# Optimization experiments

Hardware: AMD Instinct MI355X
Metric: run time of the kernel (lower is better)

## Reference

```python
import jax, jax.numpy as jnp
import numpy as np

B, C, N = 8, 3, 4096
NSAMPLE = 10
MLP = (64, 64)
# checkerboard re-gather pattern from the original module
INDS = np.array([0, 1, 2, 3, 2, 3, 4, 5, 4, 5, 6, 7, 6, 7, 8, 9])


def setup_inputs() -> dict:
    key = jax.random.key(0)
    k1, k2, k3 = jax.random.split(key, 3)
    pos = jax.random.normal(k1, (B, C, N), jnp.float32)
    w1 = jax.random.normal(k2, (MLP[0], 4 * C, 2, 2), jnp.float32) * 0.1  # Conv2d(12, mlp0, k=2)
    b1 = jnp.zeros((MLP[0],), jnp.float32)
    w2 = jax.random.normal(k3, (MLP[1], MLP[0]), jnp.float32) * 0.1       # Conv2d(mlp0, mlp1, k=1)
    b2 = jnp.zeros((MLP[1],), jnp.float32)
    return {"pos": pos, "w1": w1, "b1": b1, "w2": w2, "b2": b2}


def _squeeze_2x2_alt(x):
    # x: [B, N, c, 4, 4] -> [B, N, 4c, 2, 2] with channel order [a, d, b, c]
    a = x[..., 0::2, 0::2]  # (0,0) of each 2x2 block
    d = x[..., 1::2, 1::2]  # (1,1)
    b = x[..., 0::2, 1::2]  # (0,1)
    c = x[..., 1::2, 0::2]  # (1,0)
    return jnp.concatenate([a, d, b, c], axis=-3)


def reference(pos, w1, b1, w2, b2):
    Bn, Cn, Nn = pos.shape
    pos_t = pos.transpose(0, 2, 1)  # [B, N, C]
    # pairwise squared distances [B, N, N]
    sq = jnp.sum(pos_t * pos_t, axis=-1)
    d2 = sq[:, :, None] - 2.0 * jnp.einsum('bnc,bmc->bnm', pos_t, pos_t) + sq[:, None, :]
    _, idx = jax.lax.top_k(-d2, NSAMPLE)  # [B, N, K] nearest neighbors (self first)
    # grouping_operation: grouped[b,c,n,k] = pos[b,c,idx[b,n,k]]
    grouped = jax.vmap(lambda p, i: p[:, i])(pos, idx)  # [B, C, N, K]
    pg = grouped[..., INDS]                              # [B, C, N, 16]
    pg = pg.transpose(0, 2, 1, 3).reshape(Bn, Nn, Cn, 4, 4)  # [B, N, 3, 4, 4]
    sqz = _squeeze_2x2_alt(pg)                           # [B, N, 12, 2, 2]
    # Conv2d(12->mlp0, k=2, stride=1) over 2x2 spatial == full contraction
    h = jnp.einsum('bnchw,ochw->bno', sqz, w1) + b1      # [B, N, mlp0]
    out = jnp.einsum('bno,po->bnp', h, w2) + b2          # [B, N, mlp1]
    return out.transpose(0, 2, 1)                        # [B, mlp1, N]
```

## Files before the change

### kernel.cpp

```cpp
#include <hip/hip_runtime.h>
#include <math.h>

#define NPTS 4096
#define NSMP 10

typedef _Float16 half4 __attribute__((ext_vector_type(4)));
typedef _Float16 half8 __attribute__((ext_vector_type(8)));
typedef float f32x16 __attribute__((ext_vector_type(16)));

__global__ __launch_bounds__(256) void prep_kernel(
    const float* __restrict__ w1, const float* __restrict__ b1,
    const float* __restrict__ w2, const float* __restrict__ b2,
    float* __restrict__ wn, float* __restrict__ bb) {
  __shared__ float w1l[64 * 48];
  __shared__ float w2t[64 * 64];
  __shared__ float b1l[64];
  __shared__ float part[4][30][64];
  __shared__ float bpart[4][64];
  const int t = threadIdx.x, p = t & 63, grp = t >> 6, o0 = grp * 16;
  for (int idx = t; idx < 64 * 48; idx += 256) w1l[idx] = w1[idx];
  for (int idx = t; idx < 64 * 64; idx += 256) w2t[(idx & 63) * 64 + (idx >> 6)] = w2[idx];
  if (t < 64) b1l[t] = b1[t];
  __syncthreads();

  const int sg[16] = {0,2,4,6, 3,5,7,9, 1,3,5,7, 2,4,6,8};
  float w2r[16];
  #pragma unroll
  for (int oo = 0; oo < 16; ++oo) w2r[oo] = w2t[(o0 + oo) * 64 + p];
  float wloc[30];
  #pragma unroll
  for (int i = 0; i < 30; ++i) wloc[i] = 0.0f;
  #pragma unroll
  for (int g = 0; g < 4; ++g)
    #pragma unroll
    for (int i = 0; i < 2; ++i)
      #pragma unroll
      for (int j = 0; j < 2; ++j) {
        const int s = sg[g * 4 + i * 2 + j];
        #pragma unroll
        for (int c = 0; c < 3; ++c) {
          const int k = (c + 3 * g) * 4 + i * 2 + j;
          float wk = 0.0f;
          #pragma unroll
          for (int oo = 0; oo < 16; ++oo)
            wk = fmaf(w2r[oo], w1l[(o0 + oo) * 48 + k], wk);
          wloc[s * 3 + c] += wk;
        }
      }
  #pragma unroll
  for (int i = 0; i < 30; ++i) part[grp][i][p] = wloc[i];
  float sb = 0.0f;
  #pragma unroll
  for (int oo = 0; oo < 16; ++oo) sb = fmaf(w2r[oo], b1l[o0 + oo], sb);
  bpart[grp][p] = sb;
  __syncthreads();
  const float* p0 = &part[0][0][0];
  for (int idx = t; idx < 30 * 64; idx += 256)
    wn[idx] = p0[idx] + p0[1920 + idx] + p0[3840 + idx] + p0[5760 + idx];
  if (t < 64) bb[t] = b2[t] + bpart[0][t] + bpart[1][t] + bpart[2][t] + bpart[3][t];
}

__global__ __launch_bounds__(1024, 8) void topk_kernel(const float* __restrict__ pos,
                                                       const float* __restrict__ wng,
                                                       const float* __restrict__ bbg,
                                                       float* __restrict__ out) {
  __shared__ half4 pts4[NPTS];
  __shared__ float X[16 * 260];
  __shared__ half4 a4s[64];
  __shared__ float wl[30 * 64];
  __shared__ float bl[64];
  __shared__ float taub[64];
  __shared__ float sqqs[64];
  __shared__ int   cnt[64];
  __shared__ int   nbrT[64][NSMP];

  const int b = blockIdx.y, tid = threadIdx.x, lane = tid & 63, wv = tid >> 6;
  const float* pb = pos + (size_t)b * 3 * NPTS;
  const int nb = blockIdx.x * 64;

  for (int i = tid; i < NPTS; i += 1024) {
    float x = pb[i], y = pb[i + NPTS], z = pb[i + 2 * NPTS];
    float sq = fmaf(z, z, fmaf(y, y, x * x));
    half4 v = {(_Float16)x, (_Float16)y, (_Float16)z, (_Float16)sq};
    pts4[i] = v;
  }
  if (tid < 64) {
    float qx = pb[nb + tid], qy = pb[nb + tid + NPTS], qz = pb[nb + tid + 2 * NPTS];
    half4 va = {(_Float16)(-2.0f * (float)(_Float16)qx),
                (_Float16)(-2.0f * (float)(_Float16)qy),
                (_Float16)(-2.0f * (float)(_Float16)qz),
                (_Float16)1.0f};
    a4s[tid] = va;
    sqqs[tid] = fmaf(qz, qz, fmaf(qy, qy, qx * qx));
    cnt[tid] = 0;
    bl[tid] = bbg[tid];
  }
  for (int i = tid; i < 30 * 64; i += 1024) wl[i] = wng[i];
  __syncthreads();

  const int qt = wv >> 3, ws = wv & 7, h = lane >> 5, c31 = lane & 31;
  const int base = ws * 512;
  half8 af;
  #pragma unroll
  for (int j = 0; j < 8; ++j) af[j] = (_Float16)0.0f;
  {
    half4 aq = a4s[qt * 32 + c31];
    if (h == 0) { af[0] = aq[0]; af[1] = aq[1]; af[2] = aq[2]; af[3] = aq[3]; }
  }
  f32x16 zz;
  #pragma unroll
  for (int j = 0; j < 16; ++j) zz[j] = 0.0f;

  float mreg[16];
  #pragma unroll
  for (int j = 0; j < 16; ++j) mreg[j] = INFINITY;
  #pragma unroll 1
  for (int t = 0; t < 16; ++t) {
    half4 bp = pts4[base + t * 32 + c31];
    half8 bf;
    #pragma unroll
    for (int j = 0; j < 8; ++j) bf[j] = (_Float16)0.0f;
    bf[0] = bp[0]; bf[1] = bp[1]; bf[2] = bp[2]; bf[3] = bp[3];
    f32x16 acc = __builtin_amdgcn_mfma_f32_32x32x16_f16(af, bf, zz, 0, 0, 0);
    #pragma unroll
    for (int j = 0; j < 16; ++j) mreg[j] = fminf(mreg[j], acc[j]);
  }
  #pragma unroll
  for (int j = 0; j < 16; ++j) {
    mreg[j] = fminf(mreg[j], __shfl_xor(mreg[j], 1));
    mreg[j] = fminf(mreg[j], __shfl_xor(mreg[j], 2));
  }
  if ((lane & 3) == 0) {
    const int g = (lane >> 2) & 7;
    #pragma unroll
    for (int j = 0; j < 16; ++j) {
      const int row = qt * 32 + (j & 3) + 8 * (j >> 2) + 4 * h;
      X[row * 64 + ws * 8 + g] = mreg[j];
    }
  }
  __syncthreads();

  unsigned um[4];
  #pragma unroll
  for (int r = 0; r < 4; ++r) {
    float dm = X[(4 * wv + r) * 64 + lane];
    unsigned ub = __float_as_uint(dm);
    um[r] = (ub & 0x80000000u) ? ~ub : (ub | 0x80000000u);
  }
  unsigned pfx0 = 0u, pfx1 = 0u, pfx2 = 0u, pfx3 = 0u;
  #pragma unroll 1
  for (int bno = 31; bno >= 8; --bno) {
    const unsigned bit = 1u << bno, ones = bit - 1u;
    if (__popcll(__ballot(um[0] <= (pfx0 | ones))) < NSMP) pfx0 |= bit;
    if (__popcll(__ballot(um[1] <= (pfx1 | ones))) < NSMP) pfx1 |= bit;
    if (__popcll(__ballot(um[2] <= (pfx2 | ones))) < NSMP) pfx2 |= bit;
    if (__popcll(__ballot(um[3] <= (pfx3 | ones))) < NSMP) pfx3 |= bit;
  }
  float tx[4];
  #pragma unroll
  for (int r = 0; r < 4; ++r) {
    unsigned T = ((r == 0) ? pfx0 : (r == 1) ? pfx1 : (r == 2) ? pfx2 : pfx3) | 0xFFu;
    unsigned tb = (T & 0x80000000u) ? (T ^ 0x80000000u) : ~T;
    float tf = __uint_as_float(tb);
    float sqr = sqqs[4 * wv + r];
    float d10sq = tf + sqr;
    if (d10sq < 0.0f) d10sq = 0.0f;
    float aq = sqrtf(sqr);
    float L = aq + sqrtf(d10sq) + 0.05f;
    float slack = 2e-3f + 0.00146484375f * (4.0f * aq * L + L * L);
    tx[r] = __fadd_rn(tf, slack);
  }
  if (lane == 0) {
    taub[4 * wv + 0] = tx[0]; taub[4 * wv + 1] = tx[1];
    taub[4 * wv + 2] = tx[2]; taub[4 * wv + 3] = tx[3];
  }
  __syncthreads();

  float tau16[16];
  #pragma unroll
  for (int j = 0; j < 16; ++j) tau16[j] = taub[qt * 32 + (j & 3) + 8 * (j >> 2) + 4 * h];
  int* bufi = (int*)X;
  #pragma unroll 1
  for (int t = 0; t < 16; ++t) {
    const int m0 = base + t * 32 + c31;
    half4 bp = pts4[m0];
    half8 bf;
    #pragma unroll
    for (int j = 0; j < 8; ++j) bf[j] = (_Float16)0.0f;
    bf[0] = bp[0]; bf[1] = bp[1]; bf[2] = bp[2]; bf[3] = bp[3];
    f32x16 acc = __builtin_amdgcn_mfma_f32_32x32x16_f16(af, bf, zz, 0, 0, 0);
    #pragma unroll
    for (int j = 0; j < 16; ++j) {
      if (acc[j] <= tau16[j]) {
        const int row = qt * 32 + (j & 3) + 8 * (j >> 2) + 4 * h;
        int ps = atomicAdd(&cnt[row], 1);
        if (ps < 64) bufi[row * 64 + ps] = m0;
      }
    }
  }
  __syncthreads();

  int c[4], si[4], rank[4];
  double dd[4];
  int cmax = 0;
  #pragma unroll
  for (int r = 0; r < 4; ++r) {
    c[r] = __builtin_amdgcn_readfirstlane(cnt[4 * wv + r]);
    if (c[r] > 64) c[r] = 64;
    cmax = (c[r] > cmax) ? c[r] : cmax;
    rank[r] = 0;
  }
  #pragma unroll
  for (int r = 0; r < 4; ++r) {
    const int nq = nb + 4 * wv + r;
    float qxf = pb[nq], qyf = pb[nq + NPTS], qzf = pb[nq + 2 * NPTS];
    if (lane < c[r]) {
      si[r] = bufi[(4 * wv + r) * 64 + lane];
      float px = pb[si[r]], py = pb[si[r] + NPTS], pz = pb[si[r] + 2 * NPTS];
      double dqx = (double)qxf, dqy = (double)qyf, dqz = (double)qzf;
      double dpx = (double)px, dpy = (double)py, dpz = (double)pz;
      double dot = dqx * dpx + dqy * dpy + dqz * dpz;
      double sqn = dqx * dqx + dqy * dqy + dqz * dqz;
      double sqm = dpx * dpx + dpy * dpy + dpz * dpz;
      dd[r] = (sqn - 2.0 * dot) + sqm;
    } else { dd[r] = (double)INFINITY; si[r] = 0x7FFFFFFF; }
  }
  #pragma unroll 1
  for (int j = 0; j < cmax; ++j) {
    #pragma unroll
    for (int r = 0; r < 4; ++r) {
      int jlo = __builtin_amdgcn_readlane(__double2loint(dd[r]), j);
      int jhi = __builtin_amdgcn_readlane(__double2hiint(dd[r]), j);
      int ji  = __builtin_amdgcn_readlane(si[r], j);
      double jd = __hiloint2double(jhi, jlo);
      if (jd < dd[r] || (jd == dd[r] && ji < si[r])) ++rank[r];
    }
  }
  #pragma unroll
  for (int r = 0; r < 4; ++r)
    if (lane < c[r] && rank[r] < NSMP)
      nbrT[4 * wv + r][rank[r]] = si[r];
  __syncthreads();

  float* transF = &X[wv * 260];
  #pragma unroll 1
  for (int r = 0; r < 4; ++r) {
    float a = bl[lane];
    #pragma unroll
    for (int s = 0; s < NSMP; ++s) {
      const int id = nbrT[4 * wv + r][s];
      float px = pb[id], py = pb[id + NPTS], pz = pb[id + 2 * NPTS];
      a = fmaf(wl[(s * 3 + 0) * 64 + lane], px, a);
      a = fmaf(wl[(s * 3 + 1) * 64 + lane], py, a);
      a = fmaf(wl[(s * 3 + 2) * 64 + lane], pz, a);
    }
    transF[r * 65 + lane] = a;
  }
  __syncthreads();

  {
    int p = tid >> 4, t16 = tid & 15;
    float4 v;
    v.x = X[t16 * 260 + 0 * 65 + p];
    v.y = X[t16 * 260 + 1 * 65 + p];
    v.z = X[t16 * 260 + 2 * 65 + p];
    v.w = X[t16 * 260 + 3 * 65 + p];
    *(float4*)(out + ((size_t)b * 64 + p) * NPTS + nb + 4 * t16) = v;
  }
}

extern "C" void kernel_launch(void* const* d_in, const int* in_sizes, int n_in,
                              void* d_out, int out_size, void* d_ws, size_t ws_size,
                              hipStream_t stream) {
  (void)in_sizes; (void)n_in; (void)out_size; (void)ws_size;
  const float* pos = (const float*)d_in[0];
  const float* w1  = (const float*)d_in[1];
  const float* b1  = (const float*)d_in[2];
  const float* w2  = (const float*)d_in[3];
  const float* b2  = (const float*)d_in[4];
  float* out = (float*)d_out;

  float* wn = (float*)d_ws;
  float* bb = (float*)((char*)d_ws + 30 * 64 * 4);

  prep_kernel<<<dim3(1), dim3(256), 0, stream>>>(w1, b1, w2, b2, wn, bb);
  topk_kernel<<<dim3(64, 8), dim3(1024), 0, stream>>>(pos, wn, bb, out);
}
```

Measured before the change: 153.3 us.

## Switch distance MFMA from 32x32x16 to 16x16x32 with per-wave 16-query tiles

Replaces the 32x32x16 MFMA tiling of the query-by-point distance pass with 16x16x32 MFMAs. Each wave now covers 16 queries over a quarter of the points, with 64 iterations instead of 16, in both the min-reduction pass and the candidate collection pass. The per-lane column minimum is now written straight to a padded (stride 65) shared buffer, which drops the cross-lane shuffle reduction and is meant to reduce bank conflicts. The cost is four times as many smaller MFMA issues and more loop iterations. The minima layout changes from 8 per wave segment to 16 columns per segment, which also feeds the threshold radix search differently.

```diff
diff --git a/kernel.cpp b/kernel.cpp
--- a/kernel.cpp
+++ b/kernel.cpp
@@ -6,7 +6,7 @@
 
 typedef _Float16 half4 __attribute__((ext_vector_type(4)));
 typedef _Float16 half8 __attribute__((ext_vector_type(8)));
-typedef float f32x16 __attribute__((ext_vector_type(16)));
+typedef float f32x4 __attribute__((ext_vector_type(4)));
 
 __global__ __launch_bounds__(256) void prep_kernel(
     const float* __restrict__ w1, const float* __restrict__ b1,
@@ -98,52 +98,42 @@
   for (int i = tid; i < 30 * 64; i += 1024) wl[i] = wng[i];
   __syncthreads();
 
-  const int qt = wv >> 3, ws = wv & 7, h = lane >> 5, c31 = lane & 31;
-  const int base = ws * 512;
+  const int qt = wv >> 2, ws = wv & 3, g = lane >> 4, col = lane & 15;
+  const int base = ws * 1024;
+  const int rowb = qt * 16 + g * 4;
   half8 af;
   #pragma unroll
   for (int j = 0; j < 8; ++j) af[j] = (_Float16)0.0f;
-  {
-    half4 aq = a4s[qt * 32 + c31];
-    if (h == 0) { af[0] = aq[0]; af[1] = aq[1]; af[2] = aq[2]; af[3] = aq[3]; }
-  }
-  f32x16 zz;
-  #pragma unroll
-  for (int j = 0; j < 16; ++j) zz[j] = 0.0f;
-
-  float mreg[16];
-  #pragma unroll
-  for (int j = 0; j < 16; ++j) mreg[j] = INFINITY;
-  #pragma unroll 1
-  for (int t = 0; t < 16; ++t) {
-    half4 bp = pts4[base + t * 32 + c31];
+  if (g == 0) {
+    half4 aq = a4s[qt * 16 + col];
+    af[0] = aq[0]; af[1] = aq[1]; af[2] = aq[2]; af[3] = aq[3];
+  }
+  f32x4 zz;
+  #pragma unroll
+  for (int j = 0; j < 4; ++j) zz[j] = 0.0f;
+
+  float mreg[4];
+  #pragma unroll
+  for (int j = 0; j < 4; ++j) mreg[j] = INFINITY;
+  #pragma unroll 2
+  for (int t = 0; t < 64; ++t) {
+    half4 bp = pts4[base + t * 16 + col];
     half8 bf;
-    #pragma unroll
-    for (int j = 0; j < 8; ++j) bf[j] = (_Float16)0.0f;
     bf[0] = bp[0]; bf[1] = bp[1]; bf[2] = bp[2]; bf[3] = bp[3];
-    f32x16 acc = __builtin_amdgcn_mfma_f32_32x32x16_f16(af, bf, zz, 0, 0, 0);
-    #pragma unroll
-    for (int j = 0; j < 16; ++j) mreg[j] = fminf(mreg[j], acc[j]);
-  }
-  #pragma unroll
-  for (int j = 0; j < 16; ++j) {
-    mreg[j] = fminf(mreg[j], __shfl_xor(mreg[j], 1));
-    mreg[j] = fminf(mreg[j], __shfl_xor(mreg[j], 2));
-  }
-  if ((lane & 3) == 0) {
-    const int g = (lane >> 2) & 7;
-    #pragma unroll
-    for (int j = 0; j < 16; ++j) {
-      const int row = qt * 32 + (j & 3) + 8 * (j >> 2) + 4 * h;
-      X[row * 64 + ws * 8 + g] = mreg[j];
-    }
-  }
+    bf[4] = bp[0]; bf[5] = bp[1]; bf[6] = bp[2]; bf[7] = bp[3];
+    f32x4 acc = __builtin_amdgcn_mfma_f32_16x16x32_f16(af, bf, zz, 0, 0, 0);
+    #pragma unroll
+    for (int j = 0; j < 4; ++j) mreg[j] = fminf(mreg[j], acc[j]);
+  }
+  #pragma unroll
+  for (int j = 0; j < 4; ++j)
+    X[(rowb + j) * 65 + ws * 16 + col] = mreg[j];
   __syncthreads();
 
   unsigned um[4];
   #pragma unroll
   for (int r = 0; r < 4; ++r) {
-    float dm = X[(4 * wv + r) * 64 + lane];
+    float dm = X[(4 * wv + r) * 65 + lane];
     unsigned ub = __float_as_uint(dm);
     um[r] = (ub & 0x80000000u) ? ~ub : (ub | 0x80000000u);
   }
@@ -176,23 +166,22 @@
   }
   __syncthreads();
 
-  float tau16[16];
-  #pragma unroll
-  for (int j = 0; j < 16; ++j) tau16[j] = taub[qt * 32 + (j & 3) + 8 * (j >> 2) + 4 * h];
+  float tau4[4];
+  #pragma unroll
+  for (int j = 0; j < 4; ++j) tau4[j] = taub[rowb + j];
   int* bufi = (int*)X;
-  #pragma unroll 1
-  for (int t = 0; t < 16; ++t) {
-    const int m0 = base + t * 32 + c31;
+  #pragma unroll 2
+  for (int t = 0; t < 64; ++t) {
+    const int m0 = base + t * 16 + col;
     half4 bp = pts4[m0];
     half8 bf;
-    #pragma unroll
-    for (int j = 0; j < 8; ++j) bf[j] = (_Float16)0.0f;
     bf[0] = bp[0]; bf[1] = bp[1]; bf[2] = bp[2]; bf[3] = bp[3];
-    f32x16 acc = __builtin_amdgcn_mfma_f32_32x32x16_f16(af, bf, zz, 0, 0, 0);
-    #pragma unroll
-    for (int j = 0; j < 16; ++j) {
-      if (acc[j] <= tau16[j]) {
-        const int row = qt * 32 + (j & 3) + 8 * (j >> 2) + 4 * h;
+    bf[4] = bp[0]; bf[5] = bp[1]; bf[6] = bp[2]; bf[7] = bp[3];
+    f32x4 acc = __builtin_amdgcn_mfma_f32_16x16x32_f16(af, bf, zz, 0, 0, 0);
+    #pragma unroll
+    for (int j = 0; j < 4; ++j) {
+      if (acc[j] <= tau4[j]) {
+        const int row = rowb + j;
         int ps = atomicAdd(&cnt[row], 1);
         if (ps < 64) bufi[row * 64 + ps] = m0;
       }
```

Result: faster. 147.6 us (-3.7%).
